# Optimization experiments

Measured on AMD Instinct MI355X. Metric: run time of the kernel, lower is better.

The kernel has to match this reference:

```python
import jax, jax.numpy as jnp
import numpy as np
from jax import lax

# dims
B, K, P, S = 16, 2048, 512, 16   # batch, votes, num_proposal, nsample
C = 256                           # seed_feat_dim
RADIUS = 0.3
NH, NS, PRE, TXT = 12, 10, 256, 10
HEAD_OUT = 5 + 2 * NH + 4 * NS + PRE  # conv3 out channels = 325


def setup_inputs() -> dict:
    key = jax.random.key(0)
    ks = jax.random.split(key, 16)
    w = lambda k, shp: jax.random.normal(k, shp, jnp.float32) * 0.05
    return {
        'xyz': jax.random.normal(ks[0], (B, K, 3), jnp.float32),
        'features': jax.random.normal(ks[1], (B, C, K), jnp.float32),
        'text_feats': jax.random.normal(ks[2], (TXT, 512), jnp.float32),
        # grouping MLP (1x1 conv2d, bias folded into BN)
        'g_w0': w(ks[3], (3 + C, 128)), 'g_w1': w(ks[4], (128, 128)), 'g_w2': w(ks[5], (128, 128)),
        'g_gam0': jnp.ones(128), 'g_bet0': jnp.zeros(128),
        'g_gam1': jnp.ones(128), 'g_bet1': jnp.zeros(128),
        'g_gam2': jnp.ones(128), 'g_bet2': jnp.zeros(128),
        # decode head
        'conv1_w': w(ks[6], (128, 128)), 'conv1_b': jnp.zeros(128),
        'bn1_g': jnp.ones(128), 'bn1_b': jnp.zeros(128),
        'conv2_w': w(ks[7], (128, 128)), 'conv2_b': jnp.zeros(128),
        'bn2_g': jnp.ones(128), 'bn2_b': jnp.zeros(128),
        'conv3_w': w(ks[8], (128, HEAD_OUT)), 'conv3_b': jnp.zeros(HEAD_OUT),
        # clip header
        'h_w0': w(ks[9], (PRE, 512)), 'h_b0': jnp.zeros(512), 'h_g0': jnp.ones(512), 'h_be0': jnp.zeros(512),
        'h_w1': w(ks[10], (512, 512)), 'h_b1': jnp.zeros(512), 'h_g1': jnp.ones(512), 'h_be1': jnp.zeros(512),
        'h_w2': w(ks[11], (512, 512)), 'h_b2': jnp.zeros(512),
    }


def _fps(pts):
    # farthest point sampling of P points from pts [K,3], starting at index 0
    Kp = pts.shape[0]
    def step(carry, _):
        dmin, last = carry
        d = jnp.sum((pts - pts[last]) ** 2, -1)
        dmin = jnp.minimum(dmin, d)
        nxt = jnp.argmax(dmin).astype(jnp.int32)
        return (dmin, nxt), nxt
    d0 = jnp.full((Kp,), 1e10, pts.dtype)
    _, rest = lax.scan(step, (d0, jnp.int32(0)), None, length=P - 1)
    return jnp.concatenate([jnp.zeros((1,), jnp.int32), rest])


def _bn(x, gam, bet):
    # training-mode batchnorm over all dims but channel (last)
    ax = tuple(range(x.ndim - 1))
    m = x.mean(ax, keepdims=True)
    v = x.var(ax, keepdims=True)
    return gam * (x - m) * lax.rsqrt(v + 1e-5) + bet


def reference(xyz, features, text_feats, g_w0, g_w1, g_w2, g_gam0, g_bet0, g_gam1, g_bet1, g_gam2, g_bet2, conv1_w, conv1_b, bn1_g, bn1_b, conv2_w, conv2_b, bn2_g, bn2_b, conv3_w, conv3_b, h_w0, h_b0, h_g0, h_be0, h_w1, h_b1, h_g1, h_be1, h_w2, h_b2):
    feats_kc = features.transpose(0, 2, 1)            # [B,K,C]
    inds = jax.vmap(_fps)(xyz)                        # [B,P] int32
    new_xyz = jnp.take_along_axis(xyz, inds[..., None], axis=1)  # [B,P,3]
    # ball query: first-S in-radius indices, pad with first valid (center itself)
    d2 = jnp.sum((new_xyz[:, :, None, :] - xyz[:, None, :, :]) ** 2, -1)  # [B,P,K]
    score = jnp.where(d2 < RADIUS * RADIUS, jnp.arange(K, dtype=jnp.int32), jnp.int32(K))
    neg_vals, idx = lax.top_k(-score, S)              # smallest valid indices first
    idx = jnp.where(neg_vals > -K, idx, idx[..., :1])  # [B,P,S]
    gather = jax.vmap(lambda pts, i: pts[i])
    gx = (gather(xyz, idx) - new_xyz[:, :, None, :]) / RADIUS  # normalize_xyz
    gf = gather(feats_kc, idx)
    g = jnp.concatenate([gx, gf], -1)                 # [B,P,S,3+C] (use_xyz)
    h = jax.nn.relu(_bn(g @ g_w0, g_gam0, g_bet0))
    h = jax.nn.relu(_bn(h @ g_w1, g_gam1, g_bet1))
    h = jax.nn.relu(_bn(h @ g_w2, g_gam2, g_bet2))
    feat = h.max(axis=2)                              # [B,P,128] max-pool over neighbors
    net = jax.nn.relu(_bn(feat @ conv1_w + conv1_b, bn1_g, bn1_b))
    net = jax.nn.relu(_bn(net @ conv2_w + conv2_b, bn2_g, bn2_b))
    net = net @ conv3_w + conv3_b                     # [B,P,325]
    clip_in = net[..., -PRE:]
    hh = jax.nn.relu(_bn(clip_in @ h_w0 + h_b0, h_g0, h_be0))
    hh = jax.nn.relu(_bn(hh @ h_w1 + h_b1, h_g1, h_be1))
    q = hh @ h_w2 + h_b2                              # [B,P,512]
    q = q / jnp.linalg.norm(q, axis=-1, keepdims=True)
    t = text_feats / jnp.linalg.norm(text_feats, axis=-1, keepdims=True)
    logits = (1.0 / 0.07) * jnp.einsum('bpd,td->bpt', q, t)  # logit_scale = exp(log(1/0.07))
    out = jnp.concatenate([net[..., :-PRE], logits], -1)     # [B,P,69+TXT]
    return out.transpose(0, 2, 1)                     # [B,79,P] like torch `net`
```

## Files before the change

### kernel.cpp

```cpp
#include <hip/hip_runtime.h>
#include <hip/hip_bf16.h>
#include <cstdint>
#include <cstddef>

#define Bb 16
#define Kk 2048
#define Pp 512
#define Ss 16
#define Cc 256

typedef __attribute__((ext_vector_type(8))) short bf16x8;
typedef __attribute__((ext_vector_type(4))) float f32x4;
typedef float v2f __attribute__((ext_vector_type(2)));

__device__ __forceinline__ unsigned short f2bf(float x) {
  unsigned u = __float_as_uint(x);
  u = (u + 0x7FFF + ((u >> 16) & 1)) >> 16;
  return (unsigned short)u;
}
__device__ __forceinline__ float bf2f(unsigned short s) {
  return __uint_as_float((unsigned)s << 16);
}
__device__ __forceinline__ void split2(float x, short& h, short& l) {
  unsigned u = __float_as_uint(x);
  h = (short)(u >> 16);
  float r = x - __uint_as_float(u & 0xFFFF0000u);
  l = (short)(__float_as_uint(r) >> 16);
}

static constexpr size_t OFF_TNORM = 0;
static constexpr size_t OFF_SUMS  = 20480;
static constexpr size_t OFF_INDS  = 36864;
static constexpr size_t OFF_IDXL  = 69632;
static constexpr size_t OFF_GX    = 593920;
static constexpr size_t OFF_F1    = 2166784;
static constexpr size_t OFF_BIGA  = 18944000;
static constexpr size_t OFF_BIGB  = 86052864;
static constexpr size_t OFF_NET   = 153161728;
static constexpr size_t OFF_WTH   = 155422720;
static constexpr size_t OFF_WTL   = 156962816;

#define WT_GW1 0
#define WT_GW2 16384
#define WT_C1  32768
#define WT_C2  49152
#define WT_H0  65536
#define WT_H1  196608
#define WT_H2  458752
#define WT_C3  720896

#define SB0S 0
#define SB0Q 128
#define SB1S 256
#define SB1Q 384
#define SB2S 512
#define SB2Q 640
#define SC1S 768
#define SC1Q 896
#define SC2S 1024
#define SC2Q 1152
#define SH0S 1280
#define SH0Q 1792
#define SH1S 2304
#define SH1Q 2816

template <int CTRL>
__device__ __forceinline__ float fmax_dpp(float v) {
  int o = __builtin_amdgcn_update_dpp(0, __float_as_int(v), CTRL, 0xF, 0xF, true);
  return fmaxf(v, __int_as_float(o));
}

__global__ __launch_bounds__(256, 1) void fused_pre(
    const float* __restrict__ xyz, int* __restrict__ inds,
    const float* __restrict__ features, const float* __restrict__ g_w0,
    float* __restrict__ F1, const float* __restrict__ text,
    float* __restrict__ tn, const float* __restrict__ g_w1,
    const float* __restrict__ g_w2, const float* __restrict__ conv1_w,
    const float* __restrict__ conv2_w, const float* __restrict__ conv3_w,
    const float* __restrict__ h_w0, const float* __restrict__ h_w1,
    const float* __restrict__ h_w2, unsigned short* __restrict__ wth,
    unsigned short* __restrict__ wtl) {
  __shared__ __align__(16) float smem[8208];
  const int tid = threadIdx.x;

  if (blockIdx.x < 16) {
    #pragma clang fp contract(off)
    const int b = blockIdx.x;
    float4* pt4 = (float4*)smem;
    unsigned long long (*redw)[4] = (unsigned long long(*)[4])(smem + 8192);
    const float* base = xyz + (size_t)b * Kk * 3;
    for (int i = tid; i < Kk; i += 256) {
      pt4[i] = make_float4(base[3 * i], base[3 * i + 1], base[3 * i + 2], 0.f);
    }
    if (tid == 0) inds[b * Pp] = 0;
    v2f PX[4], PY[4], PZ[4], DM[4];
    {
      const float* pb = base + tid * 24;
      float4 f0 = *(const float4*)(pb + 0);
      float4 f1 = *(const float4*)(pb + 4);
      float4 f2 = *(const float4*)(pb + 8);
      float4 f3 = *(const float4*)(pb + 12);
      float4 f4 = *(const float4*)(pb + 16);
      float4 f5 = *(const float4*)(pb + 20);
      PX[0] = (v2f){f0.x, f0.w}; PY[0] = (v2f){f0.y, f1.x}; PZ[0] = (v2f){f0.z, f1.y};
      PX[1] = (v2f){f1.z, f2.y}; PY[1] = (v2f){f1.w, f2.z}; PZ[1] = (v2f){f2.x, f2.w};
      PX[2] = (v2f){f3.x, f3.w}; PY[2] = (v2f){f3.y, f4.x}; PZ[2] = (v2f){f3.z, f4.y};
      PX[3] = (v2f){f4.z, f5.y}; PY[3] = (v2f){f4.w, f5.z}; PZ[3] = (v2f){f5.x, f5.w};
      #pragma unroll
      for (int p = 0; p < 4; p++) DM[p] = (v2f){1e10f, 1e10f};
    }
    __syncthreads();
    const int lane = tid & 63, wid = tid >> 6;
    int last = 0;
    for (int it = 1; it < Pp; ++it) {
      float4 L = pt4[last];
      v2f vlx = {L.x, L.x}, vly = {L.y, L.y}, vlz = {L.z, L.z};
      float pf[4];
      int pk_[4];
      #pragma unroll
      for (int p = 0; p < 4; p++) {
        v2f dx = PX[p] - vlx, dy = PY[p] - vly, dz = PZ[p] - vlz;
        v2f d = (dx * dx + dy * dy) + dz * dz;
        v2f m2 = __builtin_elementwise_min(DM[p], d);
        DM[p] = m2;
        bool t = m2.y > m2.x;
        pf[p] = t ? m2.y : m2.x;
        pk_[p] = 2 * p + (t ? 1 : 0);
      }
      bool t01 = pf[1] > pf[0];
      float f01 = t01 ? pf[1] : pf[0];
      int k01 = t01 ? pk_[1] : pk_[0];
      bool t23 = pf[3] > pf[2];
      float f23 = t23 ? pf[3] : pf[2];
      int k23 = t23 ? pk_[3] : pk_[2];
      bool tt = f23 > f01;
      float bf = tt ? f23 : f01;
      int bj = tt ? k23 : k01;
      float g = bf;
      g = fmax_dpp<0xB1>(g);
      g = fmax_dpp<0x4E>(g);
      g = fmax_dpp<0x141>(g);
      g = fmax_dpp<0x140>(g);
      g = fmax_dpp<0x142>(g);
      g = fmax_dpp<0x143>(g);
      float gs = __uint_as_float(
          (unsigned)__builtin_amdgcn_readlane(__float_as_int(g), 63));
      unsigned long long msk = __ballot(bf == gs);
      int src = __builtin_ctzll(msk);
      int kk = (tid << 3) | bj;
      int kwin = __builtin_amdgcn_readlane(kk, src);
      if (lane == 0)
        redw[it & 1][wid] = ((unsigned long long)__float_as_uint(gs) << 32) |
                            (unsigned)(~(unsigned)kwin);
      __syncthreads();
      unsigned long long q0 = redw[it & 1][0], q1 = redw[it & 1][1];
      unsigned long long q2 = redw[it & 1][2], q3 = redw[it & 1][3];
      unsigned long long m0 = q0 > q1 ? q0 : q1;
      unsigned long long m1 = q2 > q3 ? q2 : q3;
      unsigned long long mm = m0 > m1 ? m0 : m1;
      last = (int)(~(unsigned)mm);
      if (tid == 0) inds[b * Pp + it] = last;
    }
  } else if (blockIdx.x == 528) {
    int w = tid >> 6, lane = tid & 63;
    for (int r = w; r < 10; r += 4) {
      const float* rw = text + (size_t)r * 512;
      float v[8];
      float ss = 0.f;
      #pragma unroll
      for (int u = 0; u < 8; u++) { v[u] = rw[lane + 64 * u]; ss += v[u] * v[u]; }
      #pragma unroll
      for (int off = 32; off; off >>= 1) ss += __shfl_xor(ss, off, 64);
      float nrm = sqrtf(ss);
      #pragma unroll
      for (int u = 0; u < 8; u++)
        tn[(size_t)r * 512 + lane + 64 * u] = v[u] / nrm;
    }
  } else if (blockIdx.x >= 529) {
    int wb = blockIdx.x - 529;
    const float* W;
    int K, N, NS, nblk, pidx;
    unsigned short *dh, *dl;
    if (wb < 4)       { W = g_w1;    K = 128; N = 128; NS = 128; dh = wth + WT_GW1; dl = wtl + WT_GW1; nblk = 4;  pidx = wb; }
    else if (wb < 8)  { W = g_w2;    K = 128; N = 128; NS = 128; dh = wth + WT_GW2; dl = wtl + WT_GW2; nblk = 4;  pidx = wb - 4; }
    else if (wb < 12) { W = conv1_w; K = 128; N = 128; NS = 128; dh = wth + WT_C1;  dl = wtl + WT_C1;  nblk = 4;  pidx = wb - 8; }
    else if (wb < 16) { W = conv2_w; K = 128; N = 128; NS = 128; dh = wth + WT_C2;  dl = wtl + WT_C2;  nblk = 4;  pidx = wb - 12; }
    else if (wb < 32) { W = h_w0;    K = 256; N = 512; NS = 512; dh = wth + WT_H0;  dl = wtl + WT_H0;  nblk = 16; pidx = wb - 16; }
    else if (wb < 64) { W = h_w1;    K = 512; N = 512; NS = 512; dh = wth + WT_H1;  dl = wtl + WT_H1;  nblk = 32; pidx = wb - 32; }
    else if (wb < 96) { W = h_w2;    K = 512; N = 512; NS = 512; dh = wth + WT_H2;  dl = wtl + WT_H2;  nblk = 32; pidx = wb - 64; }
    else              { W = conv3_w; K = 128; N = 384; NS = 325; dh = wth + WT_C3;  dl = wtl + WT_C3;  nblk = 4;  pidx = wb - 96; }
    for (int idx = pidx * 256 + tid; idx < K * N; idx += nblk * 256) {
      int k = idx / N, n = idx - k * N;
      float w = (n < NS) ? W[k * NS + n] : 0.f;
      unsigned short hi = f2bf(w);
      unsigned short lo = f2bf(w - bf2f(hi));
      dh[n * K + k] = hi;
      dl[n * K + k] = lo;
    }
  } else {
    float (*a_t)[68] = (float(*)[68])smem;
    float (*b_t)[128] = (float(*)[128])(smem + 32 * 68);
    const float* W = g_w0 + 3 * 128;
    const int m0 = (blockIdx.x - 16) * 64;
    float acc[4][8];
    #pragma unroll
    for (int i = 0; i < 4; i++)
      #pragma unroll
      for (int j = 0; j < 8; j++) acc[i][j] = 0.f;
    const int ty = tid >> 4, tx = tid & 15;
    const int lr = tid & 63, wv = tid >> 6;
    const int bb = m0 >> 11, k0 = m0 & 2047;
    const float* fb = features + (size_t)bb * (Cc * Kk);
    for (int c0 = 0; c0 < 256; c0 += 32) {
      #pragma unroll
      for (int i = 0; i < 8; i++) {
        int c = c0 + wv + 4 * i;
        a_t[wv + 4 * i][lr] = fb[(size_t)c * Kk + k0 + lr];
      }
      #pragma unroll
      for (int p = 0; p < 4; p++) {
        int cc = p * 8 + (tid >> 5);
        int nl = (tid & 31) * 4;
        *(float4*)&b_t[cc][nl] = *(const float4*)&W[(size_t)(c0 + cc) * 128 + nl];
      }
      __syncthreads();
      #pragma unroll
      for (int kk = 0; kk < 32; kk++) {
        float4 av = *(const float4*)&a_t[kk][ty * 4];
        float4 b0 = *(const float4*)&b_t[kk][tx * 4];
        float4 b1 = *(const float4*)&b_t[kk][tx * 4 + 64];
        float ap[4] = {av.x, av.y, av.z, av.w};
        float bq0[4] = {b0.x, b0.y, b0.z, b0.w};
        float bq1[4] = {b1.x, b1.y, b1.z, b1.w};
        #pragma unroll
        for (int i = 0; i < 4; i++) {
          #pragma unroll
          for (int u = 0; u < 4; u++) {
            acc[i][u] = fmaf(ap[i], bq0[u], acc[i][u]);
            acc[i][4 + u] = fmaf(ap[i], bq1[u], acc[i][4 + u]);
          }
        }
      }
      __syncthreads();
    }
    #pragma unroll
    for (int i = 0; i < 4; i++) {
      size_t mrow = (size_t)(m0 + ty * 4 + i);
      #pragma unroll
      for (int gq = 0; gq < 2; gq++) {
        float4 v4 = make_float4(acc[i][gq * 4], acc[i][gq * 4 + 1],
                                acc[i][gq * 4 + 2], acc[i][gq * 4 + 3]);
        *(float4*)&F1[mrow * 128 + gq * 64 + tx * 4] = v4;
      }
    }
  }
}

__global__ __launch_bounds__(256) void neigh_k(const float* __restrict__ xyz,
                                               const int* __restrict__ inds,
                                               int* __restrict__ idxl,
                                               float* __restrict__ gx) {
  int widx = blockIdx.x * 4 + (threadIdx.x >> 6);
  int lane = threadIdx.x & 63;
  int b = widx >> 9;
  int q = inds[widx];
  const float* base = xyz + (size_t)b * Kk * 3;
  float qx = base[3 * q], qy = base[3 * q + 1], qz = base[3 * q + 2];
  int cnt = 0;
  int myk = 0;
  for (int ch = 0; ch < 32 && cnt < Ss; ch++) {
    int k = ch * 64 + lane;
    float dx = base[3 * k] - qx;
    float dy = base[3 * k + 1] - qy;
    float dz = base[3 * k + 2] - qz;
    float d2 = __fadd_rn(__fadd_rn(__fmul_rn(dx, dx), __fmul_rn(dy, dy)),
                         __fmul_rn(dz, dz));
    unsigned long long m = __ballot(d2 < 0.09f);
    while (m && cnt < Ss) {
      int t = __builtin_ctzll(m);
      if (lane == cnt) myk = ch * 64 + t;
      cnt++;
      m &= m - 1;
    }
  }
  int first = __shfl(myk, 0, 64);
  if (lane < Ss) {
    int kk = (lane < cnt) ? myk : first;
    size_t o = (size_t)widx * Ss + lane;
    idxl[o] = kk;
    gx[o * 3 + 0] = (base[3 * kk] - qx) / 0.3f;
    gx[o * 3 + 1] = (base[3 * kk + 1] - qy) / 0.3f;
    gx[o * 3 + 2] = (base[3 * kk + 2] - qz) / 0.3f;
  }
}

template <int KD, bool INBN, bool HASBIAS, bool OSUM, bool OMAX, bool WCLIP>
__global__ __launch_bounds__(256, 2) void gemm_mfma(
    const float* __restrict__ A, const unsigned short* __restrict__ Wh,
    const unsigned short* __restrict__ Wl, const float* __restrict__ bias,
    const float* __restrict__ isum, const float* __restrict__ isq,
    float inv_cnt, const float* __restrict__ gamma,
    const float* __restrict__ beta, float* __restrict__ outp, int N, int nout,
    float* __restrict__ clipf, float* __restrict__ osum,
    float* __restrict__ osq) {
  __shared__ float sc[INBN ? KD : 1];
  __shared__ float sh[INBN ? KD : 1];
  __shared__ float red_s[OSUM ? 128 : 1];
  __shared__ float red_q[OSUM ? 128 : 1];
  const int tid = threadIdx.x;
  if (INBN) {
    for (int c = tid; c < KD; c += 256) {
      float mean = isum[c] * inv_cnt;
      float var = isq[c] * inv_cnt - mean * mean;
      float is_ = rsqrtf(var + 1e-5f);
      float scl = gamma[c] * is_;
      sc[c] = scl;
      sh[c] = beta[c] - mean * scl;
    }
  }
  if (OSUM && tid < 128) { red_s[tid] = 0.f; red_q[tid] = 0.f; }
  __syncthreads();
  const int wave = tid >> 6, lane = tid & 63;
  const int wm = wave >> 1, wn = wave & 1;
  const int r = lane & 15, g = lane >> 4;
  const size_t m0 = (size_t)blockIdx.x * 128 + wm * 64;
  const int n0 = blockIdx.y * 128 + wn * 64;

  f32x4 acc[4][4] = {};
  for (int ks = 0; ks < KD / 32; ks++) {
    const int kb = ks * 32 + g * 8;
    bf16x8 bh[4], bl[4];
    #pragma unroll
    for (int nf = 0; nf < 4; nf++) {
      bh[nf] = *(const bf16x8*)&Wh[(size_t)(n0 + nf * 16 + r) * KD + kb];
      bl[nf] = *(const bf16x8*)&Wl[(size_t)(n0 + nf * 16 + r) * KD + kb];
    }
    float s8[8], h8[8];
    if (INBN) {
      #pragma unroll
      for (int j = 0; j < 8; j++) { s8[j] = sc[kb + j]; h8[j] = sh[kb + j]; }
    }
    #pragma unroll
    for (int mf = 0; mf < 4; mf++) {
      const float* ap = &A[(m0 + mf * 16 + r) * KD + kb];
      float4 x0 = *(const float4*)ap;
      float4 x1 = *(const float4*)(ap + 4);
      float xv[8] = {x0.x, x0.y, x0.z, x0.w, x1.x, x1.y, x1.z, x1.w};
      bf16x8 ah, al;
      #pragma unroll
      for (int j = 0; j < 8; j++) {
        float x = xv[j];
        if (INBN) x = fmaxf(fmaf(x, s8[j], h8[j]), 0.f);
        short hh, ll;
        split2(x, hh, ll);
        ah[j] = hh;
        al[j] = ll;
      }
      #pragma unroll
      for (int nf = 0; nf < 4; nf++) {
        acc[mf][nf] = __builtin_amdgcn_mfma_f32_16x16x32_bf16(
            ah, bh[nf], acc[mf][nf], 0, 0, 0);
        acc[mf][nf] = __builtin_amdgcn_mfma_f32_16x16x32_bf16(
            al, bh[nf], acc[mf][nf], 0, 0, 0);
        acc[mf][nf] = __builtin_amdgcn_mfma_f32_16x16x32_bf16(
            ah, bl[nf], acc[mf][nf], 0, 0, 0);
      }
    }
  }
  float bv[4];
  if (HASBIAS) {
    #pragma unroll
    for (int nf = 0; nf < 4; nf++) {
      int col = n0 + nf * 16 + r;
      bv[nf] = (!WCLIP || col < nout) ? bias[col] : 0.f;
    }
  }
  float ps[4] = {0.f, 0.f, 0.f, 0.f}, pq[4] = {0.f, 0.f, 0.f, 0.f};
  #pragma unroll
  for (int mf = 0; mf < 4; mf++) {
    float mx[4];
    #pragma unroll
    for (int nf = 0; nf < 4; nf++) {
      float vmax = -1e30f;
      #pragma unroll
      for (int j = 0; j < 4; j++) {
        float v = acc[mf][nf][j];
        if (HASBIAS) v += bv[nf];
        size_t row = m0 + mf * 16 + g * 4 + j;
        int col = n0 + nf * 16 + r;
        if (OSUM) { ps[nf] += v; pq[nf] += v * v; }
        if (OMAX) {
          vmax = fmaxf(vmax, v);
        } else if (WCLIP) {
          if (col < 69) outp[row * 69 + col] = v;
          else if (col < nout) clipf[row * 256 + (col - 69)] = v;
        } else {
          outp[row * N + col] = v;
        }
      }
      mx[nf] = vmax;
    }
    if (OMAX) {
      #pragma unroll
      for (int nf = 0; nf < 4; nf++) {
        float m = mx[nf];
        m = fmaxf(m, __shfl_xor(m, 16, 64));
        m = fmaxf(m, __shfl_xor(m, 32, 64));
        if (g == 0) {
          size_t bq = (m0 >> 4) + mf;
          outp[bq * 128 + n0 + nf * 16 + r] = m;
        }
      }
    }
  }
  if (OSUM) {
    #pragma unroll
    for (int nf = 0; nf < 4; nf++) {
      #pragma unroll
      for (int off = 16; off < 64; off <<= 1) {
        ps[nf] += __shfl_xor(ps[nf], off, 64);
        pq[nf] += __shfl_xor(pq[nf], off, 64);
      }
    }
    if (lane < 16) {
      #pragma unroll
      for (int nf = 0; nf < 4; nf++) {
        int lcol = wn * 64 + nf * 16 + r;
        atomicAdd(&red_s[lcol], ps[nf]);
        atomicAdd(&red_q[lcol], pq[nf]);
      }
    }
    __syncthreads();
    if (tid < 128) {
      atomicAdd(&osum[blockIdx.y * 128 + tid], red_s[tid]);
      atomicAdd(&osq[blockIdx.y * 128 + tid], red_q[tid]);
    }
  }
}

__global__ __launch_bounds__(256) void gather_l1(
    const float* __restrict__ F1, const int* __restrict__ idxl,
    const float* __restrict__ gx, const float* __restrict__ g_w0,
    float* __restrict__ L1, float* __restrict__ s0, float* __restrict__ q0) {
  int col = threadIdx.x & 127, half = threadIdx.x >> 7;
  int row0 = blockIdx.x * 64 + half * 32;
  float w0 = g_w0[col], w1 = g_w0[128 + col], w2 = g_w0[256 + col];
  __shared__ float rs[128], rq[128];
  if (threadIdx.x < 128) { rs[threadIdx.x] = 0.f; rq[threadIdx.x] = 0.f; }
  __syncthreads();
  float s = 0.f, q = 0.f;
  for (int rr = 0; rr < 32; rr++) {
    int row = row0 + rr;
    int b = row >> 13;
    int idx = idxl[row];
    float g0 = gx[(size_t)row * 3], g1 = gx[(size_t)row * 3 + 1],
          g2 = gx[(size_t)row * 3 + 2];
    float v = F1[((size_t)(b * Kk + idx)) * 128 + col] + g0 * w0 + g1 * w1 +
              g2 * w2;
    L1[(size_t)row * 128 + col] = v;
    s += v;
    q += v * v;
  }
  atomicAdd(&rs[col], s);
  atomicAdd(&rq[col], q);
  __syncthreads();
  if (threadIdx.x < 128) {
    atomicAdd(&s0[threadIdx.x], rs[threadIdx.x]);
    atomicAdd(&q0[threadIdx.x], rq[threadIdx.x]);
  }
}

__global__ __launch_bounds__(512) void final2(const float* __restrict__ net,
                                              const float* __restrict__ qbuf,
                                              const float* __restrict__ tn,
                                              float* __restrict__ out) {
  __shared__ float tile[79][65];
  const int blk = blockIdx.x;
  const int tid = threadIdx.x;
  const int r = tid >> 3, oct = tid & 7;
  const int row = blk * 64 + r;
  const int b = (blk * 64) >> 9, p0 = (blk * 64) & 511;

  const float* qr = qbuf + (size_t)row * 512 + oct * 64;
  float4 q4[16];
  #pragma unroll
  for (int i = 0; i < 16; i++) q4[i] = *(const float4*)(qr + 4 * i);
  float ss = 0.f;
  float dot[10];
  #pragma unroll
  for (int t = 0; t < 10; t++) dot[t] = 0.f;
  #pragma unroll
  for (int i = 0; i < 16; i++) {
    float4 a = q4[i];
    ss += a.x * a.x + a.y * a.y + a.z * a.z + a.w * a.w;
    #pragma unroll
    for (int t = 0; t < 10; t++) {
      float4 b4 = *(const float4*)(tn + (size_t)t * 512 + oct * 64 + i * 4);
      dot[t] += a.x * b4.x + a.y * b4.y + a.z * b4.z + a.w * b4.w;
    }
  }
  #pragma unroll
  for (int off = 1; off < 8; off <<= 1) {
    ss += __shfl_xor(ss, off, 8);
    #pragma unroll
    for (int t = 0; t < 10; t++) dot[t] += __shfl_xor(dot[t], off, 8);
  }
  if (oct == 0) {
    float inv = rsqrtf(ss) * (1.f / 0.07f);
    #pragma unroll
    for (int t = 0; t < 10; t++) tile[69 + t][r] = dot[t] * inv;
  }
  for (int idx = tid; idx < 64 * 69; idx += 512) {
    int r2 = idx / 69, ch = idx - 69 * r2;
    tile[ch][r2] = net[(size_t)(blk * 64 + r2) * 69 + ch];
  }
  __syncthreads();
  for (int idx = tid; idx < 79 * 64; idx += 512) {
    int ch = idx >> 6, rr = idx & 63;
    out[((size_t)b * 79 + ch) * 512 + p0 + rr] = tile[ch][rr];
  }
}

extern "C" void kernel_launch(void* const* d_in, const int* in_sizes, int n_in,
                              void* d_out, int out_size, void* d_ws,
                              size_t ws_size, hipStream_t stream) {
  const float* xyz = (const float*)d_in[0];
  const float* features = (const float*)d_in[1];
  const float* text = (const float*)d_in[2];
  const float* g_w0 = (const float*)d_in[3];
  const float* g_w1 = (const float*)d_in[4];
  const float* g_w2 = (const float*)d_in[5];
  const float* g_gam0 = (const float*)d_in[6];
  const float* g_bet0 = (const float*)d_in[7];
  const float* g_gam1 = (const float*)d_in[8];
  const float* g_bet1 = (const float*)d_in[9];
  const float* g_gam2 = (const float*)d_in[10];
  const float* g_bet2 = (const float*)d_in[11];
  const float* conv1_w = (const float*)d_in[12];
  const float* conv1_b = (const float*)d_in[13];
  const float* bn1_g = (const float*)d_in[14];
  const float* bn1_b = (const float*)d_in[15];
  const float* conv2_w = (const float*)d_in[16];
  const float* conv2_b = (const float*)d_in[17];
  const float* bn2_g = (const float*)d_in[18];
  const float* bn2_b = (const float*)d_in[19];
  const float* conv3_w = (const float*)d_in[20];
  const float* conv3_b = (const float*)d_in[21];
  const float* h_w0 = (const float*)d_in[22];
  const float* h_b0 = (const float*)d_in[23];
  const float* h_g0 = (const float*)d_in[24];
  const float* h_be0 = (const float*)d_in[25];
  const float* h_w1 = (const float*)d_in[26];
  const float* h_b1 = (const float*)d_in[27];
  const float* h_g1 = (const float*)d_in[28];
  const float* h_be1 = (const float*)d_in[29];
  const float* h_w2 = (const float*)d_in[30];
  const float* h_b2 = (const float*)d_in[31];
  float* out = (float*)d_out;
  char* ws = (char*)d_ws;

  float* tn = (float*)(ws + OFF_TNORM);
  float* sums = (float*)(ws + OFF_SUMS);
  int* inds = (int*)(ws + OFF_INDS);
  int* idxl = (int*)(ws + OFF_IDXL);
  float* gx = (float*)(ws + OFF_GX);
  float* F1 = (float*)(ws + OFF_F1);
  float* BIGA = (float*)(ws + OFF_BIGA);
  float* BIGB = (float*)(ws + OFF_BIGB);
  float* FEAT = (float*)(ws + OFF_BIGA);
  float* C1F = (float*)(ws + OFF_BIGA + 4194304);
  float* C2F = (float*)(ws + OFF_BIGA + 8388608);
  float* CLIPF = (float*)(ws + OFF_BIGA + 12582912);
  float* H0F = (float*)(ws + OFF_BIGB);
  float* H1F = (float*)(ws + OFF_BIGB + 16777216);
  float* QF = (float*)(ws + OFF_BIGB + 33554432);
  float* net = (float*)(ws + OFF_NET);
  unsigned short* WTH = (unsigned short*)(ws + OFF_WTH);
  unsigned short* WTL = (unsigned short*)(ws + OFF_WTL);

  hipMemsetAsync(sums, 0, 16384, stream);
  fused_pre<<<629, 256, 0, stream>>>(xyz, inds, features, g_w0, F1, text, tn,
                                     g_w1, g_w2, conv1_w, conv2_w, conv3_w,
                                     h_w0, h_w1, h_w2, WTH, WTL);
  neigh_k<<<2048, 256, 0, stream>>>(xyz, inds, idxl, gx);
  gather_l1<<<2048, 256, 0, stream>>>(F1, idxl, gx, g_w0, BIGA, sums + SB0S,
                                      sums + SB0Q);
  gemm_mfma<128, true, false, true, false, false>
      <<<dim3(1024, 1), 256, 0, stream>>>(
          BIGA, WTH + WT_GW1, WTL + WT_GW1, nullptr, sums + SB0S, sums + SB0Q,
          1.f / 131072.f, g_gam0, g_bet0, BIGB, 128, 128, nullptr,
          sums + SB1S, sums + SB1Q);
  gemm_mfma<128, true, false, true, true, false>
      <<<dim3(1024, 1), 256, 0, stream>>>(
          BIGB, WTH + WT_GW2, WTL + WT_GW2, nullptr, sums + SB1S, sums + SB1Q,
          1.f / 131072.f, g_gam1, g_bet1, FEAT, 128, 128, nullptr,
          sums + SB2S, sums + SB2Q);
  gemm_mfma<128, true, true, true, false, false>
      <<<dim3(64, 1), 256, 0, stream>>>(
          FEAT, WTH + WT_C1, WTL + WT_C1, conv1_b, sums + SB2S, sums + SB2Q,
          1.f / 131072.f, g_gam2, g_bet2, C1F, 128, 128, nullptr, sums + SC1S,
          sums + SC1Q);
  gemm_mfma<128, true, true, true, false, false>
      <<<dim3(64, 1), 256, 0, stream>>>(
          C1F, WTH + WT_C2, WTL + WT_C2, conv2_b, sums + SC1S, sums + SC1Q,
          1.f / 8192.f, bn1_g, bn1_b, C2F, 128, 128, nullptr, sums + SC2S,
          sums + SC2Q);
  gemm_mfma<128, true, true, false, false, true>
      <<<dim3(64, 3), 256, 0, stream>>>(
          C2F, WTH + WT_C3, WTL + WT_C3, conv3_b, sums + SC2S, sums + SC2Q,
          1.f / 8192.f, bn2_g, bn2_b, net, 384, 325, CLIPF, nullptr, nullptr);
  gemm_mfma<256, false, true, true, false, false>
      <<<dim3(64, 4), 256, 0, stream>>>(
          CLIPF, WTH + WT_H0, WTL + WT_H0, h_b0, nullptr, nullptr, 0.f,
          nullptr, nullptr, H0F, 512, 512, nullptr, sums + SH0S, sums + SH0Q);
  gemm_mfma<512, true, true, true, false, false>
      <<<dim3(64, 4), 256, 0, stream>>>(
          H0F, WTH + WT_H1, WTL + WT_H1, h_b1, sums + SH0S, sums + SH0Q,
          1.f / 8192.f, h_g0, h_be0, H1F, 512, 512, nullptr, sums + SH1S,
          sums + SH1Q);
  gemm_mfma<512, true, true, false, false, false>
      <<<dim3(64, 4), 256, 0, stream>>>(
          H1F, WTH + WT_H2, WTL + WT_H2, h_b2, sums + SH1S, sums + SH1Q,
          1.f / 8192.f, h_g1, h_be1, QF, 512, 512, nullptr, nullptr, nullptr);
  final2<<<128, 512, 0, stream>>>(net, QF, tn, out);
}
```

Before: 784.5 us.

## Fuse neighbor gather into first grouping GEMM and store its output as bf16

```diff
diff --git a/kernel.cpp b/kernel.cpp
--- a/kernel.cpp
+++ b/kernel.cpp
@@ -256,12 +256,17 @@
   }
 }
 
-__global__ __launch_bounds__(256) void neigh_k(const float* __restrict__ xyz,
-                                               const int* __restrict__ inds,
-                                               int* __restrict__ idxl,
-                                               float* __restrict__ gx) {
-  int widx = blockIdx.x * 4 + (threadIdx.x >> 6);
-  int lane = threadIdx.x & 63;
+__global__ __launch_bounds__(256) void neigh_k(
+    const float* __restrict__ xyz, const int* __restrict__ inds,
+    const float* __restrict__ F1, const float* __restrict__ g_w0,
+    int* __restrict__ idxl, float* __restrict__ gx, float* __restrict__ s0,
+    float* __restrict__ q0) {
+  __shared__ float rs[128], rq[128];
+  const int tid = threadIdx.x;
+  if (tid < 128) { rs[tid] = 0.f; rq[tid] = 0.f; }
+  __syncthreads();
+  int widx = blockIdx.x * 4 + (tid >> 6);
+  int lane = tid & 63;
   int b = widx >> 9;
   int q = inds[widx];
   const float* base = xyz + (size_t)b * Kk * 3;
@@ -284,25 +289,58 @@
     }
   }
   int first = __shfl(myk, 0, 64);
+  int kksel = 0;
+  float g0r = 0.f, g1r = 0.f, g2r = 0.f;
   if (lane < Ss) {
     int kk = (lane < cnt) ? myk : first;
+    kksel = kk;
+    g0r = (base[3 * kk] - qx) / 0.3f;
+    g1r = (base[3 * kk + 1] - qy) / 0.3f;
+    g2r = (base[3 * kk + 2] - qz) / 0.3f;
     size_t o = (size_t)widx * Ss + lane;
     idxl[o] = kk;
-    gx[o * 3 + 0] = (base[3 * kk] - qx) / 0.3f;
-    gx[o * 3 + 1] = (base[3 * kk + 1] - qy) / 0.3f;
-    gx[o * 3 + 2] = (base[3 * kk + 2] - qz) / 0.3f;
-  }
-}
-
-template <int KD, bool INBN, bool HASBIAS, bool OSUM, bool OMAX, bool WCLIP>
+    gx[o * 3 + 0] = g0r;
+    gx[o * 3 + 1] = g1r;
+    gx[o * 3 + 2] = g2r;
+  }
+  const float* f1b = F1 + (size_t)(b << 11) * 128;
+  float wa0 = g_w0[lane], wa1 = g_w0[128 + lane], wa2 = g_w0[256 + lane];
+  float wb0 = g_w0[64 + lane], wb1 = g_w0[192 + lane], wb2 = g_w0[320 + lane];
+  float sa = 0.f, qa = 0.f, sb = 0.f, qb = 0.f;
+  #pragma unroll
+  for (int s = 0; s < Ss; s++) {
+    int bidx = __shfl(kksel, s, 64);
+    float gg0 = __shfl(g0r, s, 64);
+    float gg1 = __shfl(g1r, s, 64);
+    float gg2 = __shfl(g2r, s, 64);
+    const float* fr = f1b + (size_t)bidx * 128;
+    float va = fr[lane] + gg0 * wa0 + gg1 * wa1 + gg2 * wa2;
+    float vb = fr[64 + lane] + gg0 * wb0 + gg1 * wb1 + gg2 * wb2;
+    sa += va; qa += va * va;
+    sb += vb; qb += vb * vb;
+  }
+  atomicAdd(&rs[lane], sa);
+  atomicAdd(&rq[lane], qa);
+  atomicAdd(&rs[64 + lane], sb);
+  atomicAdd(&rq[64 + lane], qb);
+  __syncthreads();
+  if (tid < 128) {
+    atomicAdd(&s0[tid], rs[tid]);
+    atomicAdd(&q0[tid], rq[tid]);
+  }
+}
+
+template <int KD, bool INBN, bool HASBIAS, bool OSUM, bool OMAX, bool WCLIP,
+          bool ABF16, bool GATHER, bool OBF16>
 __global__ __launch_bounds__(256, 2) void gemm_mfma(
-    const float* __restrict__ A, const unsigned short* __restrict__ Wh,
+    const void* __restrict__ A, const unsigned short* __restrict__ Wh,
     const unsigned short* __restrict__ Wl, const float* __restrict__ bias,
     const float* __restrict__ isum, const float* __restrict__ isq,
     float inv_cnt, const float* __restrict__ gamma,
-    const float* __restrict__ beta, float* __restrict__ outp, int N, int nout,
+    const float* __restrict__ beta, void* __restrict__ outp, int N, int nout,
     float* __restrict__ clipf, float* __restrict__ osum,
-    float* __restrict__ osq) {
+    float* __restrict__ osq, const int* __restrict__ idxl,
+    const float* __restrict__ gxv, const float* __restrict__ w0raw) {
   __shared__ float sc[INBN ? KD : 1];
   __shared__ float sh[INBN ? KD : 1];
   __shared__ float red_s[OSUM ? 128 : 1];
@@ -326,6 +364,22 @@
   const size_t m0 = (size_t)blockIdx.x * 128 + wm * 64;
   const int n0 = blockIdx.y * 128 + wn * 64;
 
+  const float* Af = (const float*)A;
+  const unsigned short* Ab = (const unsigned short*)A;
+
+  size_t gi[4];
+  float gx0[4], gx1[4], gx2[4];
+  if (GATHER) {
+    #pragma unroll
+    for (int mf = 0; mf < 4; mf++) {
+      int row = (int)m0 + mf * 16 + r;
+      gi[mf] = ((size_t)((row >> 13) << 11) + idxl[row]) * 128;
+      gx0[mf] = gxv[3 * (size_t)row];
+      gx1[mf] = gxv[3 * (size_t)row + 1];
+      gx2[mf] = gxv[3 * (size_t)row + 2];
+    }
+  }
+
   f32x4 acc[4][4] = {};
   for (int ks = 0; ks < KD / 32; ks++) {
     const int kb = ks * 32 + g * 8;
@@ -340,12 +394,44 @@
       #pragma unroll
       for (int j = 0; j < 8; j++) { s8[j] = sc[kb + j]; h8[j] = sh[kb + j]; }
     }
+    float wxr[8], wyr[8], wzr[8];
+    if (GATHER) {
+      float4 a0 = *(const float4*)&w0raw[kb];
+      float4 a1 = *(const float4*)&w0raw[kb + 4];
+      float4 b0 = *(const float4*)&w0raw[128 + kb];
+      float4 b1 = *(const float4*)&w0raw[128 + kb + 4];
+      float4 c0 = *(const float4*)&w0raw[256 + kb];
+      float4 c1 = *(const float4*)&w0raw[256 + kb + 4];
+      wxr[0]=a0.x; wxr[1]=a0.y; wxr[2]=a0.z; wxr[3]=a0.w;
+      wxr[4]=a1.x; wxr[5]=a1.y; wxr[6]=a1.z; wxr[7]=a1.w;
+      wyr[0]=b0.x; wyr[1]=b0.y; wyr[2]=b0.z; wyr[3]=b0.w;
+      wyr[4]=b1.x; wyr[5]=b1.y; wyr[6]=b1.z; wyr[7]=b1.w;
+      wzr[0]=c0.x; wzr[1]=c0.y; wzr[2]=c0.z; wzr[3]=c0.w;
+      wzr[4]=c1.x; wzr[5]=c1.y; wzr[6]=c1.z; wzr[7]=c1.w;
+    }
     #pragma unroll
     for (int mf = 0; mf < 4; mf++) {
-      const float* ap = &A[(m0 + mf * 16 + r) * KD + kb];
-      float4 x0 = *(const float4*)ap;
-      float4 x1 = *(const float4*)(ap + 4);
-      float xv[8] = {x0.x, x0.y, x0.z, x0.w, x1.x, x1.y, x1.z, x1.w};
+      float xv[8];
+      if (GATHER) {
+        const float* fp = Af + gi[mf] + kb;
+        float4 x0 = *(const float4*)fp;
+        float4 x1 = *(const float4*)(fp + 4);
+        xv[0]=x0.x; xv[1]=x0.y; xv[2]=x0.z; xv[3]=x0.w;
+        xv[4]=x1.x; xv[5]=x1.y; xv[6]=x1.z; xv[7]=x1.w;
+        #pragma unroll
+        for (int j = 0; j < 8; j++)
+          xv[j] += gx0[mf] * wxr[j] + gx1[mf] * wyr[j] + gx2[mf] * wzr[j];
+      } else if (ABF16) {
+        bf16x8 rawv = *(const bf16x8*)&Ab[(m0 + mf * 16 + r) * KD + kb];
+        #pragma unroll
+        for (int j = 0; j < 8; j++) xv[j] = bf2f((unsigned short)rawv[j]);
+      } else {
+        const float* ap = Af + (m0 + mf * 16 + r) * KD + kb;
+        float4 x0 = *(const float4*)ap;
+        float4 x1 = *(const float4*)(ap + 4);
+        xv[0]=x0.x; xv[1]=x0.y; xv[2]=x0.z; xv[3]=x0.w;
+        xv[4]=x1.x; xv[5]=x1.y; xv[6]=x1.z; xv[7]=x1.w;
+      }
       bf16x8 ah, al;
       #pragma unroll
       for (int j = 0; j < 8; j++) {
@@ -392,10 +478,12 @@
         if (OMAX) {
           vmax = fmaxf(vmax, v);
         } else if (WCLIP) {
-          if (col < 69) outp[row * 69 + col] = v;
+          if (col < 69) ((float*)outp)[row * 69 + col] = v;
           else if (col < nout) clipf[row * 256 + (col - 69)] = v;
+        } else if (OBF16) {
+          ((unsigned short*)outp)[row * N + col] = f2bf(v);
         } else {
-          outp[row * N + col] = v;
+          ((float*)outp)[row * N + col] = v;
         }
       }
       mx[nf] = vmax;
@@ -408,7 +496,7 @@
         m = fmaxf(m, __shfl_xor(m, 32, 64));
         if (g == 0) {
           size_t bq = (m0 >> 4) + mf;
-          outp[bq * 128 + n0 + nf * 16 + r] = m;
+          ((float*)outp)[bq * 128 + n0 + nf * 16 + r] = m;
         }
       }
     }
@@ -435,38 +523,6 @@
       atomicAdd(&osum[blockIdx.y * 128 + tid], red_s[tid]);
       atomicAdd(&osq[blockIdx.y * 128 + tid], red_q[tid]);
     }
-  }
-}
-
-__global__ __launch_bounds__(256) void gather_l1(
-    const float* __restrict__ F1, const int* __restrict__ idxl,
-    const float* __restrict__ gx, const float* __restrict__ g_w0,
-    float* __restrict__ L1, float* __restrict__ s0, float* __restrict__ q0) {
-  int col = threadIdx.x & 127, half = threadIdx.x >> 7;
-  int row0 = blockIdx.x * 64 + half * 32;
-  float w0 = g_w0[col], w1 = g_w0[128 + col], w2 = g_w0[256 + col];
-  __shared__ float rs[128], rq[128];
-  if (threadIdx.x < 128) { rs[threadIdx.x] = 0.f; rq[threadIdx.x] = 0.f; }
-  __syncthreads();
-  float s = 0.f, q = 0.f;
-  for (int rr = 0; rr < 32; rr++) {
-    int row = row0 + rr;
-    int b = row >> 13;
-    int idx = idxl[row];
-    float g0 = gx[(size_t)row * 3], g1 = gx[(size_t)row * 3 + 1],
-          g2 = gx[(size_t)row * 3 + 2];
-    float v = F1[((size_t)(b * Kk + idx)) * 128 + col] + g0 * w0 + g1 * w1 +
-              g2 * w2;
-    L1[(size_t)row * 128 + col] = v;
-    s += v;
-    q += v * v;
-  }
-  atomicAdd(&rs[col], s);
-  atomicAdd(&rq[col], q);
-  __syncthreads();
-  if (threadIdx.x < 128) {
-    atomicAdd(&s0[threadIdx.x], rs[threadIdx.x]);
-    atomicAdd(&q0[threadIdx.x], rq[threadIdx.x]);
   }
 }
 
@@ -565,15 +621,14 @@
   int* idxl = (int*)(ws + OFF_IDXL);
   float* gx = (float*)(ws + OFF_GX);
   float* F1 = (float*)(ws + OFF_F1);
-  float* BIGA = (float*)(ws + OFF_BIGA);
-  float* BIGB = (float*)(ws + OFF_BIGB);
-  float* FEAT = (float*)(ws + OFF_BIGA);
-  float* C1F = (float*)(ws + OFF_BIGA + 4194304);
-  float* C2F = (float*)(ws + OFF_BIGA + 8388608);
-  float* CLIPF = (float*)(ws + OFF_BIGA + 12582912);
-  float* H0F = (float*)(ws + OFF_BIGB);
-  float* H1F = (float*)(ws + OFF_BIGB + 16777216);
-  float* QF = (float*)(ws + OFF_BIGB + 33554432);
+  unsigned short* L2OUT = (unsigned short*)(ws + OFF_BIGA);
+  float* QF = (float*)(ws + OFF_BIGA);
+  float* FEAT = (float*)(ws + OFF_BIGB);
+  float* C1F = (float*)(ws + OFF_BIGB + 4194304);
+  float* C2F = (float*)(ws + OFF_BIGB + 8388608);
+  float* CLIPF = (float*)(ws + OFF_BIGB + 12582912);
+  float* H0F = (float*)(ws + OFF_BIGB + 20971520);
+  float* H1F = (float*)(ws + OFF_BIGB + 37748736);
   float* net = (float*)(ws + OFF_NET);
   unsigned short* WTH = (unsigned short*)(ws + OFF_WTH);
   unsigned short* WTL = (unsigned short*)(ws + OFF_WTL);
@@ -582,45 +637,47 @@
   fused_pre<<<629, 256, 0, stream>>>(xyz, inds, features, g_w0, F1, text, tn,
                                      g_w1, g_w2, conv1_w, conv2_w, conv3_w,
                                      h_w0, h_w1, h_w2, WTH, WTL);
-  neigh_k<<<2048, 256, 0, stream>>>(xyz, inds, idxl, gx);
-  gather_l1<<<2048, 256, 0, stream>>>(F1, idxl, gx, g_w0, BIGA, sums + SB0S,
-                                      sums + SB0Q);
-  gemm_mfma<128, true, false, true, false, false>
+  neigh_k<<<2048, 256, 0, stream>>>(xyz, inds, F1, g_w0, idxl, gx,
+                                    sums + SB0S, sums + SB0Q);
+  gemm_mfma<128, true, false, true, false, false, false, true, true>
       <<<dim3(1024, 1), 256, 0, stream>>>(
-          BIGA, WTH + WT_GW1, WTL + WT_GW1, nullptr, sums + SB0S, sums + SB0Q,
-          1.f / 131072.f, g_gam0, g_bet0, BIGB, 128, 128, nullptr,
-          sums + SB1S, sums + SB1Q);
-  gemm_mfma<128, true, false, true, true, false>
+          F1, WTH + WT_GW1, WTL + WT_GW1, nullptr, sums + SB0S, sums + SB0Q,
+          1.f / 131072.f, g_gam0, g_bet0, L2OUT, 128, 128, nullptr,
+          sums + SB1S, sums + SB1Q, idxl, gx, g_w0);
+  gemm_mfma<128, true, false, true, true, false, true, false, false>
       <<<dim3(1024, 1), 256, 0, stream>>>(
-          BIGB, WTH + WT_GW2, WTL + WT_GW2, nullptr, sums + SB1S, sums + SB1Q,
-          1.f / 131072.f, g_gam1, g_bet1, FEAT, 128, 128, nullptr,
-          sums + SB2S, sums + SB2Q);
-  gemm_mfma<128, true, true, true, false, false>
+          L2OUT, WTH + WT_GW2, WTL + WT_GW2, nullptr, sums + SB1S,
+          sums + SB1Q, 1.f / 131072.f, g_gam1, g_bet1, FEAT, 128, 128,
+          nullptr, sums + SB2S, sums + SB2Q, nullptr, nullptr, nullptr);
+  gemm_mfma<128, true, true, true, false, false, false, false, false>
       <<<dim3(64, 1), 256, 0, stream>>>(
           FEAT, WTH + WT_C1, WTL + WT_C1, conv1_b, sums + SB2S, sums + SB2Q,
           1.f / 131072.f, g_gam2, g_bet2, C1F, 128, 128, nullptr, sums + SC1S,
-          sums + SC1Q);
-  gemm_mfma<128, true, true, true, false, false>
+          sums + SC1Q, nullptr, nullptr, nullptr);
+  gemm_mfma<128, true, true, true, false, false, false, false, false>
       <<<dim3(64, 1), 256, 0, stream>>>(
           C1F, WTH + WT_C2, WTL + WT_C2, conv2_b, sums + SC1S, sums + SC1Q,
           1.f / 8192.f, bn1_g, bn1_b, C2F, 128, 128, nullptr, sums + SC2S,
-          sums + SC2Q);
-  gemm_mfma<128, true, true, false, false, true>
+          sums + SC2Q, nullptr, nullptr, nullptr);
+  gemm_mfma<128, true, true, false, false, true, false, false, false>
       <<<dim3(64, 3), 256, 0, stream>>>(
           C2F, WTH + WT_C3, WTL + WT_C3, conv3_b, sums + SC2S, sums + SC2Q,
-          1.f / 8192.f, bn2_g, bn2_b, net, 384, 325, CLIPF, nullptr, nullptr);
-  gemm_mfma<256, false, true, true, false, false>
+          1.f / 8192.f, bn2_g, bn2_b, net, 384, 325, CLIPF, nullptr, nullptr,
+          nullptr, nullptr, nullptr);
+  gemm_mfma<256, false, true, true, false, false, false, false, false>
       <<<dim3(64, 4), 256, 0, stream>>>(
           CLIPF, WTH + WT_H0, WTL + WT_H0, h_b0, nullptr, nullptr, 0.f,
-          nullptr, nullptr, H0F, 512, 512, nullptr, sums + SH0S, sums + SH0Q);
-  gemm_mfma<512, true, true, true, false, false>
+          nullptr, nullptr, H0F, 512, 512, nullptr, sums + SH0S, sums + SH0Q,
+          nullptr, nullptr, nullptr);
+  gemm_mfma<512, true, true, true, false, false, false, false, false>
       <<<dim3(64, 4), 256, 0, stream>>>(
           H0F, WTH + WT_H1, WTL + WT_H1, h_b1, sums + SH0S, sums + SH0Q,
           1.f / 8192.f, h_g0, h_be0, H1F, 512, 512, nullptr, sums + SH1S,
-          sums + SH1Q);
-  gemm_mfma<512, true, true, false, false, false>
+          sums + SH1Q, nullptr, nullptr, nullptr);
+  gemm_mfma<512, true, true, false, false, false, false, false, false>
       <<<dim3(64, 4), 256, 0, stream>>>(
           H1F, WTH + WT_H2, WTL + WT_H2, h_b2, sums + SH1S, sums + SH1Q,
-          1.f / 8192.f, h_g1, h_be1, QF, 512, 512, nullptr, nullptr, nullptr);
+          1.f / 8192.f, h_g1, h_be1, QF, 512, 512, nullptr, nullptr, nullptr,
+          nullptr, nullptr, nullptr);
   final2<<<128, 512, 0, stream>>>(net, QF, tn, out);
 }
```

New measurement: 749.7 us. 4.4% less time.
